# Kernel optimization log

Measured on AMD Instinct MI355X. Metric: run time of the kernel, lower is better.

Reference implementation:

```python
import jax, jax.numpy as jnp
import numpy as np

NS = [65536, 16384, 4096, 1024, 256, 64]          # nodes per level (64 = 8 graphs x 8 dense voxels)
ES = [1048576, 262144, 65536, 16384, 4096]        # edges per level (avg degree 16)
INS = [1, 15, 23, 31, 39]
OUTS = [12, 20, 28, 36, 44]
K = 5                                             # kernel_size


def setup_inputs():
    keys = iter(jax.random.split(jax.random.key(0), 64))
    d = {'x': jax.random.normal(next(keys), (NS[0], 1), jnp.float32),
         'pos': jax.random.uniform(next(keys), (NS[0], 3), jnp.float32)}
    for l in range(5):
        n, e, ci, co = NS[l], ES[l], INS[l], OUTS[l]
        d[f'src{l}'] = jax.random.randint(next(keys), (e,), 0, n)
        d[f'dst{l}'] = jax.random.randint(next(keys), (e,), 0, n)
        d[f'eattr{l}'] = jax.random.normal(next(keys), (e, 3), jnp.float32)
        d[f'cluster{l}'] = jax.random.randint(next(keys), (n,), 0, NS[l + 1])
        d[f'w1_{l}'] = jax.random.normal(next(keys), (3, K), jnp.float32) * 0.5
        d[f'b1_{l}'] = jnp.zeros((K,), jnp.float32)
        d[f'w2_{l}'] = jax.random.normal(next(keys), (K, ci * co), jnp.float32) / np.float32(np.sqrt(K * ci))
        d[f'b2_{l}'] = jnp.zeros((ci * co,), jnp.float32)
        d[f'root_{l}'] = jax.random.normal(next(keys), (ci, co), jnp.float32) / np.float32(np.sqrt(ci))
        d[f'bias_{l}'] = jnp.zeros((co,), jnp.float32)
    d['fc_w'] = jax.random.normal(next(keys), (8 * 47, 10), jnp.float32) / np.float32(np.sqrt(8 * 47))
    d['fc_b'] = jnp.zeros((10,), jnp.float32)
    return d


def _conv(x, src, dst, eattr, w1, b1, w2, b2, root, bias, n):
    # edge-conditioned kernel: MLP(edge_attr) -> [E, ci, co]
    h = jnp.tanh(eattr @ w1 + b1)                                  # [E, K]
    We = (h @ w2 + b2).reshape(eattr.shape[0], x.shape[1], -1)     # [E, ci, co]
    msg = jnp.einsum('ei,eio->eo', x[src], We)                     # gather + per-edge matvec
    s = jax.ops.segment_sum(msg, dst, num_segments=n)
    cnt = jax.ops.segment_sum(jnp.ones((dst.shape[0], 1), x.dtype), dst, num_segments=n)
    agg = s / jnp.maximum(cnt, 1.0)                                # mean aggregation
    return agg + x @ root + bias, jnp.mean(jnp.square(We))


def _pool(x, pos, cluster, n_next):
    # sparse voxel max pool on features, mean on positions; pos concatenated to features
    xm = jax.ops.segment_max(x, cluster, num_segments=n_next)
    xm = jnp.where(jnp.isfinite(xm), xm, 0.0)                      # empty voxels -> 0
    ps = jax.ops.segment_sum(pos, cluster, num_segments=n_next)
    cnt = jax.ops.segment_sum(jnp.ones((pos.shape[0], 1), pos.dtype), cluster, num_segments=n_next)
    pm = ps / jnp.maximum(cnt, 1.0)
    return jnp.concatenate([xm, pm], axis=1), pm


def reference(x, pos, src0, dst0, eattr0, cluster0, w1_0, b1_0, w2_0, b2_0, root_0, bias_0,
              src1, dst1, eattr1, cluster1, w1_1, b1_1, w2_1, b2_1, root_1, bias_1,
              src2, dst2, eattr2, cluster2, w1_2, b1_2, w2_2, b2_2, root_2, bias_2,
              src3, dst3, eattr3, cluster3, w1_3, b1_3, w2_3, b2_3, root_3, bias_3,
              src4, dst4, eattr4, cluster4, w1_4, b1_4, w2_4, b2_4, root_4, bias_4,
              fc_w, fc_b):
    lv = [(src0, dst0, eattr0, cluster0, w1_0, b1_0, w2_0, b2_0, root_0, bias_0),
          (src1, dst1, eattr1, cluster1, w1_1, b1_1, w2_1, b2_1, root_1, bias_1),
          (src2, dst2, eattr2, cluster2, w1_2, b1_2, w2_2, b2_2, root_2, bias_2),
          (src3, dst3, eattr3, cluster3, w1_3, b1_3, w2_3, b2_3, root_3, bias_3),
          (src4, dst4, eattr4, cluster4, w1_4, b1_4, w2_4, b2_4, root_4, bias_4)]
    closs = jnp.float32(0.0)
    for l, (src, dst, ea, cl, w1, b1, w2, b2, rt, bs) in enumerate(lv):
        x, c = _conv(x, src, dst, ea, w1, b1, w2, b2, rt, bs, NS[l])
        closs = closs + c
        x, pos = _pool(x, pos, cl, NS[l + 1])
    feat = x.reshape(-1, 8 * 47)                                   # [B, 8*47]
    logits = feat @ fc_w + fc_b
    return jax.nn.log_softmax(logits, axis=1), closs
```

## Files before the change

kernel.cpp:

```cpp
#include <hip/hip_runtime.h>
#include <hip/hip_fp16.h>
#include <math.h>


#define NBUCK 8
#define TILES0 256
#define NB0    512
#define IDXCAP 3072
#define TILES1 64
#define NB1    512

struct SegArgs {
    const int* idx[10];
    int*       cnt[10];
    int*       rp [10];
    int*       out[10];
    int        n  [10];
    int        nb [10];
    int        shift[10];
    int        tstart[11];
};

struct ScanAux {
    int* tilesum;
    int* tileoff;
    int  sstart[11];
    int  T;
};

struct HArgs {
    const float* eattr[5];
    const float* w1[5];
    const float* b1[5];
    float*       H;
    int          E[5];
    int          bstart[6];
};

struct WArgs {
    const float* w2[5];
    const float* b2[5];
    const float* H;
    float*       sq;
    int          cico[5];
    int          E[5];
};

__global__ __launch_bounds__(256) void countA_k(
    SegArgs a, HArgs ha, const int* __restrict__ dst0,
    const int* __restrict__ dst1, int* __restrict__ M, int* __restrict__ M1,
    int histBlocks)
{
    __shared__ int sh[NB0];
    int B = blockIdx.x;
    int t = threadIdx.x;

    if (B < TILES0) {
        for (int u = t; u < NB0; u += 256) sh[u] = 0;
        __syncthreads();
        int base = B * 4096 + t;
        #pragma unroll
        for (int it = 0; it < 16; it++)
            atomicAdd(&sh[dst0[base + it * 256] >> 7], 1);
        __syncthreads();
        for (int u = t; u < NB0; u += 256) M[(size_t)B * NB0 + u] = sh[u];
        return;
    }
    B -= TILES0;
    if (B < TILES1) {
        for (int u = t; u < NB1; u += 256) sh[u] = 0;
        __syncthreads();
        int base = B * 4096 + t;
        #pragma unroll
        for (int it = 0; it < 16; it++)
            atomicAdd(&sh[dst1[base + it * 256] >> 5], 1);
        __syncthreads();
        for (int u = t; u < NB1; u += 256) M1[(size_t)B * NB1 + u] = sh[u];
        return;
    }
    B -= TILES1;
    if (B < histBlocks) {
        int bucket = B % NBUCK;
        int T = B / NBUCK;
        int s = 0;
        while (s < 9 && T >= a.tstart[s + 1]) s++;
        int i = (T - a.tstart[s]) * 256 + t;
        if (i >= a.n[s]) return;
        int d = a.idx[s][i];
        if ((d >> a.shift[s]) != bucket) return;
        atomicAdd(&a.cnt[s][d], 1);
        return;
    }
    int b = B - histBlocks;
    const int K = 32;
    int l = 0;
    while (l < 4 && b >= ha.bstart[l + 1]) l++;
    int bloc = b - ha.bstart[l];
    const float* ea = ha.eattr[l];
    float w1r[15], b1r[5];
    #pragma unroll
    for (int i = 0; i < 15; i++) w1r[i] = ha.w1[l][i];
    #pragma unroll
    for (int i = 0; i < 5; i++)  b1r[i] = ha.b1[l][i];
    float acc[20];
    #pragma unroll
    for (int i = 0; i < 20; i++) acc[i] = 0.f;
    int base = bloc * 256 * K + t;
    for (int it = 0; it < K; it++) {
        int e = base + it * 256;
        if (e < ha.E[l]) {
            float e0 = ea[e * 3], e1 = ea[e * 3 + 1], e2 = ea[e * 3 + 2];
            float h[5];
            #pragma unroll
            for (int k = 0; k < 5; k++)
                h[k] = tanhf(e0 * w1r[k] + e1 * w1r[5 + k] + e2 * w1r[10 + k] + b1r[k]);
            int p = 5;
            #pragma unroll
            for (int k = 0; k < 5; k++) {
                acc[k] += h[k];
                #pragma unroll
                for (int k2 = k; k2 < 5; k2++) acc[p++] += h[k] * h[k2];
            }
        }
    }
    float* red = (float*)sh;
    int wid = t >> 6, lane = t & 63;
    #pragma unroll
    for (int v = 0; v < 20; v++) {
        float s = acc[v];
        #pragma unroll
        for (int o = 32; o; o >>= 1) s += __shfl_down(s, o);
        if (lane == 0) red[wid * 20 + v] = s;
    }
    __syncthreads();
    if (t < 20)
        atomicAdd(&ha.H[l * 20 + t],
                  red[t] + red[20 + t] + red[40 + t] + red[60 + t]);
}

__global__ __launch_bounds__(256) void scanP1_k(
    SegArgs a, ScanAux x, const int* __restrict__ M, int* __restrict__ M2,
    int* __restrict__ colTotal, const int* __restrict__ M1,
    int* __restrict__ M21, int* __restrict__ ct1)
{
    __shared__ int sc[256];
    int B = blockIdx.x;
    int t = threadIdx.x;

    if (B < NB0) {
        int v = M[(size_t)t * NB0 + B];
        sc[t] = v;
        __syncthreads();
        for (int d = 1; d < 256; d <<= 1) {
            int u = (t >= d) ? sc[t - d] : 0;
            __syncthreads();
            sc[t] += u;
            __syncthreads();
        }
        M2[(size_t)t * NB0 + B] = sc[t] - v;
        if (t == 255) colTotal[B] = sc[255];
        return;
    }
    B -= NB0;
    if (B < NB1) {
        if (t >= 64) return;
        int v = M1[(size_t)t * NB1 + B];
        int val = v;
        #pragma unroll
        for (int d = 1; d < 64; d <<= 1) {
            int u = __shfl_up(val, d);
            if (t >= d) val += u;
        }
        M21[(size_t)t * NB1 + B] = val - v;
        if (t == 63) ct1[B] = val;
        return;
    }
    int b = B - NB1;
    int s = 0;
    while (s < 9 && b >= x.sstart[s + 1]) s++;
    int tloc = b - x.sstart[s];
    int nb = a.nb[s];
    const int* cnt = a.cnt[s];
    int i0 = tloc * 4096 + t * 16;
    int sum = 0;
    #pragma unroll
    for (int k = 0; k < 16; k++) {
        int i = i0 + k;
        if (i < nb) sum += cnt[i];
    }
    #pragma unroll
    for (int o = 32; o; o >>= 1) sum += __shfl_down(sum, o);
    if ((t & 63) == 0) sc[t >> 6] = sum;
    __syncthreads();
    if (t == 0)
        x.tilesum[b] = sc[0] + sc[1] + sc[2] + sc[3];
}

__global__ __launch_bounds__(512) void scanP2_k(
    SegArgs a, ScanAux x, const int* __restrict__ colTotal,
    int* __restrict__ bucketStart, const int* __restrict__ ct1,
    int* __restrict__ bs1)
{
    __shared__ int sc[NB0];
    int t = threadIdx.x;
    if (blockIdx.x == 0) {
        int v = colTotal[t];
        sc[t] = v;
        __syncthreads();
        for (int d = 1; d < NB0; d <<= 1) {
            int u = (t >= d) ? sc[t - d] : 0;
            __syncthreads();
            sc[t] += u;
            __syncthreads();
        }
        bucketStart[t] = sc[t] - v;
        if (t == NB0 - 1) bucketStart[NB0] = sc[NB0 - 1];
        return;
    }
    if (blockIdx.x == 2) {
        int v = ct1[t];
        sc[t] = v;
        __syncthreads();
        for (int d = 1; d < NB1; d <<= 1) {
            int u = (t >= d) ? sc[t - d] : 0;
            __syncthreads();
            sc[t] += u;
            __syncthreads();
        }
        bs1[t] = sc[t] - v;
        if (t == NB1 - 1) bs1[NB1] = sc[NB1 - 1];
        return;
    }
    if (t >= 64) return;
    int lane = t;
    int orig = (lane < x.T) ? x.tilesum[lane] : 0;
    int val = orig;
    #pragma unroll
    for (int d = 1; d < 64; d <<= 1) {
        int v = __shfl_up(val, d);
        if (lane >= d) val += v;
    }
    int excl = val - orig;
    int s = 0;
    while (s < 9 && lane >= x.sstart[s + 1]) s++;
    int segExcl = __shfl(excl, x.sstart[s]);
    if (lane < x.T) {
        x.tileoff[lane] = excl - segExcl;
        if (lane == x.sstart[s + 1] - 1)
            a.rp[s][a.nb[s]] = val - segExcl;
    }
}

__global__ __launch_bounds__(256) void scanP3_k(
    SegArgs a, ScanAux x,
    const int* __restrict__ src, const int* __restrict__ dst,
    const float* __restrict__ ea, const float* __restrict__ x0,
    const int* __restrict__ M2, const int* __restrict__ bucketStart,
    float4* __restrict__ pay2,
    const float* __restrict__ w1, const float* __restrict__ b1,
    float* __restrict__ H0,
    const int* __restrict__ src1, const int* __restrict__ dst1,
    const float* __restrict__ ea1, const int* __restrict__ M21,
    const int* __restrict__ bs1, float4* __restrict__ pay1)
{
    __shared__ int   shi[NB0];
    __shared__ float shf[100];
    int B = blockIdx.x;
    int t = threadIdx.x;

    if (B < x.T) {
        int s = 0;
        while (s < 9 && B >= x.sstart[s + 1]) s++;
        int tloc = B - x.sstart[s];
        int nb = a.nb[s];
        const int* cnt = a.cnt[s];
        int* rp = a.rp[s];
        int i0 = tloc * 4096 + t * 16;
        int v[16];
        int sum = 0;
        #pragma unroll
        for (int k = 0; k < 16; k++) {
            int i = i0 + k;
            v[k] = (i < nb) ? cnt[i] : 0;
            sum += v[k];
        }
        int acc = sum;
        shi[t] = acc;
        __syncthreads();
        for (int d = 1; d < 256; d <<= 1) {
            int t2 = (t >= d) ? shi[t - d] : 0;
            __syncthreads();
            acc += t2;
            shi[t] = acc;
            __syncthreads();
        }
        int running = x.tileoff[B] + (acc - sum);
        #pragma unroll
        for (int k = 0; k < 16; k++) {
            int i = i0 + k;
            if (i < nb) rp[i] = running;
            running += v[k];
        }
        return;
    }
    B -= x.T;
    if (B < TILES0) {
        int tile = B;
        for (int u = t; u < NB0; u += 256)
            shi[u] = bucketStart[u] + M2[(size_t)tile * NB0 + u];
        if (t < 15) shf[t] = w1[t];
        if (t >= 32 && t < 37) shf[15 + t - 32] = b1[t - 32];
        __syncthreads();

        float acc[20];
        #pragma unroll
        for (int i = 0; i < 20; i++) acc[i] = 0.f;

        int base = tile * 4096 + t;
        #pragma unroll 4
        for (int it = 0; it < 16; it++) {
            int i = base + it * 256;
            int d = dst[i];
            float e0 = ea[i * 3], e1 = ea[i * 3 + 1], e2 = ea[i * 3 + 2];
            float h[5];
            #pragma unroll
            for (int k = 0; k < 5; k++)
                h[k] = tanhf(e0 * shf[k] + e1 * shf[5 + k] + e2 * shf[10 + k] + shf[15 + k]);
            int p = 5;
            #pragma unroll
            for (int k = 0; k < 5; k++) {
                acc[k] += h[k];
                #pragma unroll
                for (int k2 = k; k2 < 5; k2++) acc[p++] += h[k] * h[k2];
            }
            float xv = x0[src[i]];
            union HU { __half2 h2; float f; } p01, p23;
            p01.h2 = __floats2half2_rn(h[0], h[1]);
            p23.h2 = __floats2half2_rn(h[2], h[3]);
            unsigned wbits = ((unsigned)d << 16) |
                             (unsigned)__half_as_ushort(__float2half_rn(h[4]));
            int ps = atomicAdd(&shi[d >> 7], 1);
            pay2[ps] = make_float4(xv, p01.f, p23.f, __uint_as_float(wbits));
        }

        int wid = t >> 6, lane = t & 63;
        #pragma unroll
        for (int v = 0; v < 20; v++) {
            float s = acc[v];
            #pragma unroll
            for (int o = 32; o; o >>= 1) s += __shfl_down(s, o);
            if (lane == 0) shf[20 + wid * 20 + v] = s;
        }
        __syncthreads();
        if (t < 20)
            atomicAdd(&H0[t], shf[20 + t] + shf[40 + t] + shf[60 + t] + shf[80 + t]);
        return;
    }
    int tile = B - TILES0;
    for (int u = t; u < NB1; u += 256)
        shi[u] = bs1[u] + M21[(size_t)tile * NB1 + u];
    __syncthreads();
    int base = tile * 4096 + t;
    #pragma unroll 4
    for (int it = 0; it < 16; it++) {
        int i = base + it * 256;
        int d = dst1[i];
        int key = (d << 16) | src1[i];
        float e0 = ea1[i * 3], e1 = ea1[i * 3 + 1], e2 = ea1[i * 3 + 2];
        int ps = atomicAdd(&shi[d >> 5], 1);
        pay1[ps] = make_float4(__int_as_float(key), e0, e1, e2);
    }
}

__global__ __launch_bounds__(256) void scatC_k(
    SegArgs a, WArgs wa, int histBlocks,
    const float4* __restrict__ pay2, const int* __restrict__ bucketStart,
    const float* __restrict__ w2, const float* __restrict__ b2,
    const float* __restrict__ root, const float* __restrict__ bias,
    const float* __restrict__ x, float* __restrict__ y,
    const float4* __restrict__ pay1, const int* __restrict__ bs1,
    int* __restrict__ rp1, float4* __restrict__ rec1)
{
    __shared__ float wsm[96];
    __shared__ int hist[128], st[128], cur[128];
    __shared__ int idxL[IDXCAP];
    int B = blockIdx.x;
    int t = threadIdx.x;

    if (B < histBlocks) {
        int bucket = B % NBUCK;
        int T = B / NBUCK;
        int s = 0;
        while (s < 9 && T >= a.tstart[s + 1]) s++;
        int i = (T - a.tstart[s]) * 256 + t;
        if (i >= a.n[s]) return;
        int d = a.idx[s][i];
        if ((d >> a.shift[s]) != bucket) return;
        int p = atomicSub(&a.cnt[s][d], 1) - 1;
        a.out[s][a.rp[s][d] + p] = i;
        return;
    }
    B -= histBlocks;
    if (B < NB0) {
        if (t < 60) wsm[t] = w2[t];
        else if (t >= 64  && t < 76)  wsm[60 + t - 64]  = b2[t - 64];
        else if (t >= 128 && t < 140) wsm[72 + t - 128] = root[t - 128];
        else if (t >= 192 && t < 204) wsm[84 + t - 192] = bias[t - 192];
        if (t < 128) hist[t] = 0;
        __syncthreads();

        int lo = bucketStart[B], hi = bucketStart[B + 1];
        int bin0 = B << 7;
        const float* payw = (const float*)pay2;
        for (int j = lo + t; j < hi; j += 256) {
            int rel = (int)(__float_as_uint(payw[4 * j + 3]) >> 16) - bin0;
            atomicAdd(&hist[rel], 1);
        }
        __syncthreads();
        if (t < 128) st[t] = hist[t];
        __syncthreads();
        for (int d = 1; d < 128; d <<= 1) {
            int u = (t < 128 && t >= d) ? st[t - d] : 0;
            __syncthreads();
            if (t < 128) st[t] += u;
            __syncthreads();
        }
        if (t < 128) cur[t] = st[t] - hist[t];
        __syncthreads();
        for (int j = lo + t; j < hi; j += 256) {
            int rel = (int)(__float_as_uint(payw[4 * j + 3]) >> 16) - bin0;
            int p = atomicAdd(&cur[rel], 1);
            idxL[p] = j;
        }
        __syncthreads();

        if (t < 128) {
            int v = bin0 + t;
            int deg = hist[t];
            int s0 = st[t] - deg;
            float S0 = 0.f, S1 = 0.f, S2 = 0.f, S3 = 0.f, S4 = 0.f, S5 = 0.f;
            for (int jj = s0; jj < s0 + deg; jj++) {
                float4 R = pay2[idxL[jj]];
                union HU { float f; __half2 h2; } a01, a23;
                a01.f = R.y; a23.f = R.z;
                unsigned wbits = __float_as_uint(R.w);
                float xv = R.x;
                S0 += xv;
                S1 += __low2float(a01.h2)  * xv;
                S2 += __high2float(a01.h2) * xv;
                S3 += __low2float(a23.h2)  * xv;
                S4 += __high2float(a23.h2) * xv;
                S5 += __half2float(__ushort_as_half((unsigned short)(wbits & 0xffffu))) * xv;
            }
            float inv = 1.f / fmaxf((float)deg, 1.f);
            float xv = x[v];
            #pragma unroll
            for (int o = 0; o < 12; o++) {
                float msg = wsm[60 + o] * S0 + wsm[o] * S1 + wsm[12 + o] * S2 +
                            wsm[24 + o] * S3 + wsm[36 + o] * S4 + wsm[48 + o] * S5;
                y[v * 12 + o] = msg * inv + xv * wsm[72 + o] + wsm[84 + o];
            }
        }
        return;
    }
    B -= NB0;
    if (B < 5) {
        if (t >= 64) return;
        int l = B;
        const float* w2l = wa.w2[l];
        const float* b2l = wa.b2[l];
        int cico = wa.cico[l];
        float d[21];
        #pragma unroll
        for (int i = 0; i < 21; i++) d[i] = 0.f;
        for (int u = t; u < cico; u += 64) {
            float b = b2l[u];
            float w[5];
            #pragma unroll
            for (int k = 0; k < 5; k++) w[k] = w2l[k * cico + u];
            int p = 0;
            #pragma unroll
            for (int k = 0; k < 5; k++) {
                #pragma unroll
                for (int k2 = k; k2 < 5; k2++) d[p++] += w[k] * w[k2];
            }
            #pragma unroll
            for (int k = 0; k < 5; k++) d[15 + k] += b * w[k];
            d[20] += b * b;
        }
        #pragma unroll
        for (int i = 0; i < 21; i++) {
            #pragma unroll
            for (int off = 32; off; off >>= 1) d[i] += __shfl_down(d[i], off);
        }
        if (t == 0) {
            const float* H1 = wa.H + l * 20;
            const float* H2 = H1 + 5;
            float sq = (float)wa.E[l] * d[20];
            #pragma unroll
            for (int k = 0; k < 5; k++) sq += 2.f * d[15 + k] * H1[k];
            int p = 0;
            #pragma unroll
            for (int k = 0; k < 5; k++) {
                #pragma unroll
                for (int k2 = k; k2 < 5; k2++) {
                    sq += ((k == k2) ? 1.f : 2.f) * d[p] * H2[p];
                    p++;
                }
            }
            wa.sq[l] = sq;
        }
        return;
    }
    int b = B - 5;
    int lo = bs1[b], hi = bs1[b + 1];
    int bin0 = b << 5;
    if (t < 32) hist[t] = 0;
    __syncthreads();
    const float* payw = (const float*)pay1;
    for (int j = lo + t; j < hi; j += 256) {
        int rel = (int)(__float_as_uint(payw[4 * j]) >> 16) - bin0;
        atomicAdd(&hist[rel], 1);
    }
    __syncthreads();
    if (t < 32) {
        int v = hist[t];
        int val = v;
        #pragma unroll
        for (int d = 1; d < 32; d <<= 1) {
            int u = __shfl_up(val, d);
            if (t >= d) val += u;
        }
        st[t] = val - v;
        cur[t] = lo + val - v;
        rp1[bin0 + t] = lo + val - v;
        if (b == NB1 - 1 && t == 31) rp1[NB1 * 32] = hi;
    }
    __syncthreads();
    for (int j = lo + t; j < hi; j += 256) {
        float4 R = pay1[j];
        int rel = (int)(__float_as_uint(R.x) >> 16) - bin0;
        int p = atomicAdd(&cur[rel], 1);
        rec1[p] = R;
    }
}

__global__ __launch_bounds__(256) void conv1s_k(
    const int* __restrict__ rp, const float4* __restrict__ rec,
    const float* __restrict__ w1, const float* __restrict__ b1,
    const float* __restrict__ w2, const float* __restrict__ b2,
    const float* __restrict__ root, const float* __restrict__ bias,
    const float* __restrict__ x, float* __restrict__ y)
{
    constexpr int CI = 15, CO = 20, CH = 48, CICO = CI * CO;
    __shared__ float w1s[20];
    __shared__ float4 recb[CH];
    __shared__ int   svb[CH];
    __shared__ float hb[CH * 6];
    __shared__ float xs[CH * CI];
    __shared__ float S[6 * CI];

    int t = threadIdx.x;
    int v = blockIdx.x;
    if (t < 20) w1s[t] = (t < 15) ? w1[t] : b1[t - 15];
    int r0 = rp[v], r1 = rp[v + 1];
    int d  = r1 - r0;
    float acc = 0.f;

    for (int c0 = r0; c0 < r1; c0 += CH) {
        int cn = min(CH, r1 - c0);
        if (t < cn) {
            float4 R = rec[c0 + t];
            recb[t] = R;
            svb[t]  = (int)(__float_as_uint(R.x) & 0xffffu);
            hb[t * 6] = 1.f;
        }
        __syncthreads();
        if (t < cn * 5) {
            int j = t / 5, k = t % 5;
            float e0 = recb[j].y, e1 = recb[j].z, e2 = recb[j].w;
            hb[j * 6 + 1 + k] =
                tanhf(e0 * w1s[k] + e1 * w1s[5 + k] + e2 * w1s[10 + k] + w1s[15 + k]);
        }
        for (int u = t; u < cn * CI; u += 256)
            xs[u] = x[(size_t)svb[u / CI] * CI + (u % CI)];
        __syncthreads();
        if (t < 6 * CI) {
            int i = t / 6, k6 = t % 6;
            for (int j = 0; j < cn; j++)
                acc += hb[j * 6 + k6] * xs[j * CI + i];
        }
        __syncthreads();
    }

    if (t < 6 * CI) S[t] = acc;
    __syncthreads();

    if (t < CO) {
        float m = 0.f;
        for (int i = 0; i < CI; i++) {
            m += b2[i * CO + t] * S[i * 6];
            #pragma unroll
            for (int k = 0; k < 5; k++)
                m += w2[k * CICO + i * CO + t] * S[i * 6 + 1 + k];
        }
        m /= fmaxf((float)d, 1.f);
        for (int i = 0; i < CI; i++)
            m += x[(size_t)v * CI + i] * root[i * CO + t];
        y[(size_t)v * CO + t] = m + bias[t];
    }
}

template<int CI, int CO>
__global__ __launch_bounds__(256) void coop_conv_k(
    const int* __restrict__ rp, const int* __restrict__ eid,
    const int* __restrict__ src, const float* __restrict__ eattr,
    const float* __restrict__ w1, const float* __restrict__ b1,
    const float* __restrict__ w2, const float* __restrict__ b2,
    const float* __restrict__ root, const float* __restrict__ bias,
    const float* __restrict__ x, float* __restrict__ y)
{
    constexpr int CH   = 48;
    constexpr int CICO = CI * CO;
    __shared__ float w1s[20];
    __shared__ int   eb[CH], svb[CH];
    __shared__ float hb[CH * 6];
    __shared__ float xs[CH * CI];
    __shared__ float S[6 * CI];

    int t = threadIdx.x;
    int v = blockIdx.x;
    if (t < 20) w1s[t] = (t < 15) ? w1[t] : b1[t - 15];
    int r0 = rp[v], r1 = rp[v + 1];
    int d  = r1 - r0;
    float acc = 0.f;

    for (int c0 = r0; c0 < r1; c0 += CH) {
        int cn = min(CH, r1 - c0);
        if (t < cn) {
            int e = eid[c0 + t];
            eb[t]  = e;
            svb[t] = src[e];
            hb[t * 6] = 1.f;
        }
        __syncthreads();
        if (t < cn * 5) {
            int j = t / 5, k = t % 5;
            int e = eb[j];
            float e0 = eattr[e * 3], e1 = eattr[e * 3 + 1], e2 = eattr[e * 3 + 2];
            hb[j * 6 + 1 + k] =
                tanhf(e0 * w1s[k] + e1 * w1s[5 + k] + e2 * w1s[10 + k] + w1s[15 + k]);
        }
        for (int u = t; u < cn * CI; u += 256)
            xs[u] = x[(size_t)svb[u / CI] * CI + (u % CI)];
        __syncthreads();
        if (t < 6 * CI) {
            int i = t / 6, k6 = t % 6;
            for (int j = 0; j < cn; j++)
                acc += hb[j * 6 + k6] * xs[j * CI + i];
        }
        __syncthreads();
    }

    if (t < 6 * CI) S[t] = acc;
    __syncthreads();

    if (t < CO) {
        float m = 0.f;
        for (int i = 0; i < CI; i++) {
            m += b2[i * CO + t] * S[i * 6];
            #pragma unroll
            for (int k = 0; k < 5; k++)
                m += w2[k * CICO + i * CO + t] * S[i * 6 + 1 + k];
        }
        m /= fmaxf((float)d, 1.f);
        for (int i = 0; i < CI; i++)
            m += x[(size_t)v * CI + i] * root[i * CO + t];
        y[(size_t)v * CO + t] = m + bias[t];
    }
}

template<int CO>
__global__ __launch_bounds__(256) void pool_k(
    int NN,
    const int* __restrict__ crp, const int* __restrict__ cnid,
    const float* __restrict__ y, const float* __restrict__ pos,
    float* __restrict__ xn, float* __restrict__ pn)
{
    int t = blockIdx.x * 256 + threadIdx.x;
    if (t >= NN * (CO + 3)) return;
    int c = t / (CO + 3), o = t % (CO + 3);
    int r0 = crp[c], r1 = crp[c + 1];
    int d = r1 - r0;
    if (o < CO) {
        float m = -INFINITY;
        for (int j = r0; j < r1; j++)
            m = fmaxf(m, y[(size_t)cnid[j] * CO + o]);
        if (d == 0 || !isfinite(m)) m = 0.f;
        xn[c * (CO + 3) + o] = m;
    } else {
        int k = o - CO;
        float sum = 0.f;
        for (int j = r0; j < r1; j++)
            sum += pos[cnid[j] * 3 + k];
        float pm = sum / fmaxf((float)d, 1.f);
        xn[c * (CO + 3) + CO + k] = pm;
        pn[c * 3 + k] = pm;
    }
}

__global__ __launch_bounds__(128) void fc_k(
    const float* __restrict__ x5,
    const float* __restrict__ fc_w, const float* __restrict__ fc_b,
    const float* __restrict__ sq, float* __restrict__ out)
{
    __shared__ float feat[8 * 376];
    __shared__ float logit[80];
    __shared__ float roff[8];
    for (int t = threadIdx.x; t < 8 * 376; t += 128) feat[t] = x5[t];
    __syncthreads();
    int t = threadIdx.x;
    if (t < 80) {
        int b = t / 10, j = t % 10;
        float acc = fc_b[j];
        for (int k = 0; k < 376; k++) acc += feat[b * 376 + k] * fc_w[k * 10 + j];
        logit[t] = acc;
    }
    __syncthreads();
    if (t < 8) {
        float m = -1e30f;
        for (int j = 0; j < 10; j++) m = fmaxf(m, logit[t * 10 + j]);
        float ssum = 0.f;
        for (int j = 0; j < 10; j++) ssum += expf(logit[t * 10 + j] - m);
        roff[t] = m + logf(ssum);
    }
    __syncthreads();
    if (t < 80) out[t] = logit[t] - roff[t / 10];
    if (t == 0) {
        float closs = 0.f;
        closs += sq[0] * (1.0f / 12582912.0f);
        closs += sq[1] * (1.0f / 78643200.0f);
        closs += sq[2] * (1.0f / 42205184.0f);
        closs += sq[3] * (1.0f / 18284544.0f);
        closs += sq[4] * (1.0f / 7028736.0f);
        out[80] = closs;
    }
}


extern "C" void kernel_launch(void* const* d_in, const int* in_sizes, int n_in,
                              void* d_out, int out_size, void* d_ws, size_t ws_size,
                              hipStream_t stream)
{
    static const int NSa[6] = {65536, 16384, 4096, 1024, 256, 64};
    static const int ESa[5] = {1048576, 262144, 65536, 16384, 4096};
    static const int COa[5] = {12, 20, 28, 36, 44};
    static const int CIa[5] = {1, 15, 23, 31, 39};

    const float* x0   = (const float*)d_in[0];
    const float* pos0 = (const float*)d_in[1];

    int* wsw = (int*)d_ws;
    size_t off = 0;
    auto alw = [&](size_t n) -> size_t {
        size_t p = off; off += (n + 63) & ~(size_t)63; return p;
    };
    size_t degO[5], cdegO[5];
    for (int l = 2; l < 5; l++) degO[l]  = alw(NSa[l]);
    for (int l = 0; l < 5; l++) cdegO[l] = alw(NSa[l + 1]);
    size_t HO = alw(100);
    size_t zeroWords = off;
    size_t rpO[5], crpO[5], eidO[5], cnidO[5];
    rpO[1] = alw(NSa[1] + 1);
    for (int l = 2; l < 5; l++) rpO[l]  = alw(NSa[l] + 1);
    for (int l = 0; l < 5; l++) crpO[l] = alw(NSa[l + 1] + 1);
    for (int l = 2; l < 5; l++) eidO[l] = alw(ESa[l]);
    for (int l = 0; l < 5; l++) cnidO[l] = alw(NSa[l]);
    size_t tsO  = alw(64);
    size_t toO  = alw(64);
    size_t MO   = alw((size_t)TILES0 * NB0);
    size_t M2O  = alw((size_t)TILES0 * NB0);
    size_t ctO  = alw(NB0);
    size_t bsO  = alw(NB0 + 1);
    size_t payO = alw((size_t)ESa[0] * 4);
    size_t M1O  = alw((size_t)TILES1 * NB1);
    size_t M21O = alw((size_t)TILES1 * NB1);
    size_t ct1O = alw(NB1);
    size_t bs1O = alw(NB1 + 1);
    size_t pay1O = alw((size_t)ESa[1] * 4);
    size_t rec1O = alw((size_t)ESa[1] * 4);
    size_t yO   = alw((size_t)65536 * 12);
    size_t sqO  = alw(8);
    size_t xnO[5], pnO[5];
    for (int l = 0; l < 5; l++) xnO[l] = alw((size_t)NSa[l + 1] * (COa[l] + 3));
    for (int l = 0; l < 5; l++) pnO[l] = alw((size_t)NSa[l + 1] * 3);

    hipMemsetAsync(d_ws, 0, zeroWords * 4, stream);

    SegArgs sa{};
    int nseg = 0;
    for (int l = 2; l < 5; l++) {
        sa.idx[nseg] = (const int*)d_in[3 + 10 * l];
        sa.cnt[nseg] = wsw + degO[l];
        sa.rp [nseg] = wsw + rpO[l];
        sa.out[nseg] = wsw + eidO[l];
        sa.n  [nseg] = ESa[l];
        sa.nb [nseg] = NSa[l];
        nseg++;
    }
    for (int l = 0; l < 5; l++) {
        sa.idx[nseg] = (const int*)d_in[5 + 10 * l];
        sa.cnt[nseg] = wsw + cdegO[l];
        sa.rp [nseg] = wsw + crpO[l];
        sa.out[nseg] = wsw + cnidO[l];
        sa.n  [nseg] = NSa[l];
        sa.nb [nseg] = NSa[l + 1];
        nseg++;
    }
    ScanAux sx{};
    int tiles = 0, btiles = 0;
    for (int s = 0; s < nseg; s++) {
        int lg = 31 - __builtin_clz(sa.nb[s]);
        sa.shift[s] = lg - 3;
        sa.tstart[s] = tiles;
        tiles += (sa.n[s] + 255) / 256;
        sx.sstart[s] = btiles;
        btiles += (sa.nb[s] + 4095) / 4096;
    }
    for (int s = nseg; s <= 10; s++) {
        sa.tstart[s] = tiles;
        sx.sstart[s] = btiles;
        if (s < 10) {
            sa.idx[s] = sa.idx[nseg - 1]; sa.cnt[s] = sa.cnt[nseg - 1];
            sa.rp[s] = sa.rp[nseg - 1];   sa.out[s] = sa.out[nseg - 1];
            sa.n[s] = 0; sa.nb[s] = 8; sa.shift[s] = 0;
        }
    }
    sx.T = btiles;
    sx.tilesum = wsw + tsO;
    sx.tileoff = wsw + toO;
    int histBlocks = tiles * NBUCK;

    float4* pay2 = (float4*)(wsw + payO);
    float4* pay1 = (float4*)(wsw + pay1O);
    float4* rec1 = (float4*)(wsw + rec1O);
    float*  Hp   = (float*)(wsw + HO);

    HArgs ha{};
    int bs = 0;
    ha.bstart[0] = 0;
    ha.eattr[0] = (const float*)d_in[4];
    ha.w1[0] = (const float*)d_in[6];
    ha.b1[0] = (const float*)d_in[7];
    ha.E[0] = 0;
    for (int l = 1; l < 5; l++) {
        ha.eattr[l] = (const float*)d_in[4 + 10 * l];
        ha.w1[l]    = (const float*)d_in[6 + 10 * l];
        ha.b1[l]    = (const float*)d_in[7 + 10 * l];
        ha.E[l]     = ESa[l];
        ha.bstart[l] = bs;
        bs += (ESa[l] + 256 * 32 - 1) / (256 * 32);
    }
    ha.bstart[5] = bs;
    ha.H = Hp;

    WArgs wa{};
    for (int l = 0; l < 5; l++) {
        wa.w2[l]   = (const float*)d_in[8 + 10 * l];
        wa.b2[l]   = (const float*)d_in[9 + 10 * l];
        wa.cico[l] = CIa[l] * COa[l];
        wa.E[l]    = ESa[l];
    }
    wa.H  = Hp;
    wa.sq = (float*)(wsw + sqO);

    countA_k<<<TILES0 + TILES1 + histBlocks + bs, 256, 0, stream>>>(
        sa, ha, (const int*)d_in[3], (const int*)d_in[13],
        wsw + MO, wsw + M1O, histBlocks);
    scanP1_k<<<NB0 + NB1 + btiles, 256, 0, stream>>>(
        sa, sx, wsw + MO, wsw + M2O, wsw + ctO,
        wsw + M1O, wsw + M21O, wsw + ct1O);
    scanP2_k<<<3, 512, 0, stream>>>(sa, sx, wsw + ctO, wsw + bsO,
                                    wsw + ct1O, wsw + bs1O);
    scanP3_k<<<btiles + TILES0 + TILES1, 256, 0, stream>>>(
        sa, sx,
        (const int*)d_in[2], (const int*)d_in[3], (const float*)d_in[4],
        x0, wsw + M2O, wsw + bsO, pay2,
        (const float*)d_in[6], (const float*)d_in[7], Hp,
        (const int*)d_in[12], (const int*)d_in[13], (const float*)d_in[14],
        wsw + M21O, wsw + bs1O, pay1);

    float* yb = (float*)(wsw + yO);

    scatC_k<<<histBlocks + NB0 + 5 + NB1, 256, 0, stream>>>(
        sa, wa, histBlocks, pay2, wsw + bsO,
        (const float*)d_in[8], (const float*)d_in[9],
        (const float*)d_in[10], (const float*)d_in[11], x0, yb,
        pay1, wsw + bs1O, wsw + rpO[1], rec1);

    pool_k<12><<<(NSa[1] * 15 + 255) / 256, 256, 0, stream>>>(
        NSa[1], wsw + crpO[0], wsw + cnidO[0], yb, pos0,
        (float*)(wsw + xnO[0]), (float*)(wsw + pnO[0]));

    conv1s_k<<<NSa[1], 256, 0, stream>>>(
        wsw + rpO[1], rec1,
        (const float*)d_in[16], (const float*)d_in[17],
        (const float*)d_in[18], (const float*)d_in[19],
        (const float*)d_in[20], (const float*)d_in[21],
        (const float*)(wsw + xnO[0]), yb);
    pool_k<20><<<(NSa[2] * 23 + 255) / 256, 256, 0, stream>>>(
        NSa[2], wsw + crpO[1], wsw + cnidO[1], yb,
        (const float*)(wsw + pnO[0]),
        (float*)(wsw + xnO[1]), (float*)(wsw + pnO[1]));

#define LVLC(l, CI_, CO_) do {                                                 \
    const float* xin   = (const float*)(wsw + xnO[(l) - 1]);                   \
    const float* posin = (const float*)(wsw + pnO[(l) - 1]);                   \
    int N = NSa[(l)], NN = NSa[(l) + 1];                                       \
    coop_conv_k<CI_, CO_><<<N, 256, 0, stream>>>(                              \
        wsw + rpO[(l)], wsw + eidO[(l)],                                       \
        (const int*)d_in[2 + 10 * (l)], (const float*)d_in[4 + 10 * (l)],      \
        (const float*)d_in[6 + 10 * (l)], (const float*)d_in[7 + 10 * (l)],    \
        (const float*)d_in[8 + 10 * (l)], (const float*)d_in[9 + 10 * (l)],    \
        (const float*)d_in[10 + 10 * (l)], (const float*)d_in[11 + 10 * (l)],  \
        xin, yb);                                                              \
    pool_k<CO_><<<(NN * ((CO_) + 3) + 255) / 256, 256, 0, stream>>>(           \
        NN, wsw + crpO[(l)], wsw + cnidO[(l)], yb, posin,                      \
        (float*)(wsw + xnO[(l)]), (float*)(wsw + pnO[(l)]));                   \
} while (0)

    LVLC(2, 23, 28);
    LVLC(3, 31, 36);
    LVLC(4, 39, 44);
#undef LVLC

    fc_k<<<1, 128, 0, stream>>>((const float*)(wsw + xnO[4]),
                                (const float*)d_in[52], (const float*)d_in[53],
                                wa.sq, (float*)d_out);
}
```

Baseline: 416.5 us.

## Retile count/scatter phases, drop bucketed histograms, use LDS atomics for level-0 aggregation

Shrinks the per-block tiles in the level-0/1 bucket counting and payload scatter from 4096 to 1024 edges, giving more blocks, and makes the scan pass read four tile rows per thread. The 8-way bucket-filtered segment histogram and fill passes become a single pass with direct global atomics. Level-0 aggregation now accumulates straight into shared-memory float atomics instead of building a per-node local index list. tanhf is replaced by an exp-based fast tanh, and block orders inside the fused kernels are rearranged. These changes cut redundant reads and serial per-node loops, but they add atomic contention and make float summation order nondeterministic.

```diff
diff --git a/kernel.cpp b/kernel.cpp
--- a/kernel.cpp
+++ b/kernel.cpp
@@ -3,12 +3,17 @@
 #include <math.h>
 
 
-#define NBUCK 8
-#define TILES0 256
+#define TILES0 1024
+#define TSZ0   1024
 #define NB0    512
-#define IDXCAP 3072
-#define TILES1 64
+#define TILES1 256
+#define TSZ1   1024
 #define NB1    512
+
+__device__ __forceinline__ float ftanh(float x) {
+    float e = __expf(2.f * x);
+    return 1.f - 2.f / (e + 1.f);
+}
 
 struct SegArgs {
     const int* idx[10];
@@ -17,7 +22,6 @@
     int*       out[10];
     int        n  [10];
     int        nb [10];
-    int        shift[10];
     int        tstart[11];
 };
 
@@ -49,7 +53,7 @@
 __global__ __launch_bounds__(256) void countA_k(
     SegArgs a, HArgs ha, const int* __restrict__ dst0,
     const int* __restrict__ dst1, int* __restrict__ M, int* __restrict__ M1,
-    int histBlocks)
+    int hsBlocks)
 {
     __shared__ int sh[NB0];
     int B = blockIdx.x;
@@ -58,9 +62,9 @@
     if (B < TILES0) {
         for (int u = t; u < NB0; u += 256) sh[u] = 0;
         __syncthreads();
-        int base = B * 4096 + t;
-        #pragma unroll
-        for (int it = 0; it < 16; it++)
+        int base = B * TSZ0 + t;
+        #pragma unroll
+        for (int it = 0; it < 4; it++)
             atomicAdd(&sh[dst0[base + it * 256] >> 7], 1);
         __syncthreads();
         for (int u = t; u < NB0; u += 256) M[(size_t)B * NB0 + u] = sh[u];
@@ -70,72 +74,76 @@
     if (B < TILES1) {
         for (int u = t; u < NB1; u += 256) sh[u] = 0;
         __syncthreads();
-        int base = B * 4096 + t;
-        #pragma unroll
-        for (int it = 0; it < 16; it++)
+        int base = B * TSZ1 + t;
+        #pragma unroll
+        for (int it = 0; it < 4; it++)
             atomicAdd(&sh[dst1[base + it * 256] >> 5], 1);
         __syncthreads();
         for (int u = t; u < NB1; u += 256) M1[(size_t)B * NB1 + u] = sh[u];
         return;
     }
     B -= TILES1;
-    if (B < histBlocks) {
-        int bucket = B % NBUCK;
-        int T = B / NBUCK;
+    if (B < hsBlocks) {
+        const int K = 8;
+        int l = 0;
+        while (l < 4 && B >= ha.bstart[l + 1]) l++;
+        int bloc = B - ha.bstart[l];
+        const float* ea = ha.eattr[l];
+        float w1r[15], b1r[5];
+        #pragma unroll
+        for (int i = 0; i < 15; i++) w1r[i] = ha.w1[l][i];
+        #pragma unroll
+        for (int i = 0; i < 5; i++)  b1r[i] = ha.b1[l][i];
+        float acc[20];
+        #pragma unroll
+        for (int i = 0; i < 20; i++) acc[i] = 0.f;
+        int base = bloc * 256 * K + t;
+        for (int it = 0; it < K; it++) {
+            int e = base + it * 256;
+            if (e < ha.E[l]) {
+                float e0 = ea[e * 3], e1 = ea[e * 3 + 1], e2 = ea[e * 3 + 2];
+                float h[5];
+                #pragma unroll
+                for (int k = 0; k < 5; k++)
+                    h[k] = ftanh(e0 * w1r[k] + e1 * w1r[5 + k] + e2 * w1r[10 + k] + b1r[k]);
+                int p = 5;
+                #pragma unroll
+                for (int k = 0; k < 5; k++) {
+                    acc[k] += h[k];
+                    #pragma unroll
+                    for (int k2 = k; k2 < 5; k2++) acc[p++] += h[k] * h[k2];
+                }
+            }
+        }
+        float* red = (float*)sh;
+        int wid = t >> 6, lane = t & 63;
+        #pragma unroll
+        for (int v = 0; v < 20; v++) {
+            float s = acc[v];
+            #pragma unroll
+            for (int o = 32; o; o >>= 1) s += __shfl_down(s, o);
+            if (lane == 0) red[wid * 20 + v] = s;
+        }
+        __syncthreads();
+        if (t < 20)
+            atomicAdd(&ha.H[l * 20 + t],
+                      red[t] + red[20 + t] + red[40 + t] + red[60 + t]);
+        return;
+    }
+    B -= hsBlocks;
+    {
         int s = 0;
-        while (s < 9 && T >= a.tstart[s + 1]) s++;
-        int i = (T - a.tstart[s]) * 256 + t;
-        if (i >= a.n[s]) return;
-        int d = a.idx[s][i];
-        if ((d >> a.shift[s]) != bucket) return;
-        atomicAdd(&a.cnt[s][d], 1);
-        return;
-    }
-    int b = B - histBlocks;
-    const int K = 32;
-    int l = 0;
-    while (l < 4 && b >= ha.bstart[l + 1]) l++;
-    int bloc = b - ha.bstart[l];
-    const float* ea = ha.eattr[l];
-    float w1r[15], b1r[5];
-    #pragma unroll
-    for (int i = 0; i < 15; i++) w1r[i] = ha.w1[l][i];
-    #pragma unroll
-    for (int i = 0; i < 5; i++)  b1r[i] = ha.b1[l][i];
-    float acc[20];
-    #pragma unroll
-    for (int i = 0; i < 20; i++) acc[i] = 0.f;
-    int base = bloc * 256 * K + t;
-    for (int it = 0; it < K; it++) {
-        int e = base + it * 256;
-        if (e < ha.E[l]) {
-            float e0 = ea[e * 3], e1 = ea[e * 3 + 1], e2 = ea[e * 3 + 2];
-            float h[5];
-            #pragma unroll
-            for (int k = 0; k < 5; k++)
-                h[k] = tanhf(e0 * w1r[k] + e1 * w1r[5 + k] + e2 * w1r[10 + k] + b1r[k]);
-            int p = 5;
-            #pragma unroll
-            for (int k = 0; k < 5; k++) {
-                acc[k] += h[k];
-                #pragma unroll
-                for (int k2 = k; k2 < 5; k2++) acc[p++] += h[k] * h[k2];
-            }
-        }
-    }
-    float* red = (float*)sh;
-    int wid = t >> 6, lane = t & 63;
-    #pragma unroll
-    for (int v = 0; v < 20; v++) {
-        float s = acc[v];
-        #pragma unroll
-        for (int o = 32; o; o >>= 1) s += __shfl_down(s, o);
-        if (lane == 0) red[wid * 20 + v] = s;
-    }
-    __syncthreads();
-    if (t < 20)
-        atomicAdd(&ha.H[l * 20 + t],
-                  red[t] + red[20 + t] + red[40 + t] + red[60 + t]);
+        while (s < 9 && B >= a.tstart[s + 1]) s++;
+        int i0 = (B - a.tstart[s]) * 1024;
+        const int* idx = a.idx[s];
+        int* cnt = a.cnt[s];
+        int n = a.n[s];
+        #pragma unroll
+        for (int j = 0; j < 4; j++) {
+            int i = i0 + j * 256 + t;
+            if (i < n) atomicAdd(&cnt[idx[i]], 1);
+        }
+    }
 }
 
 __global__ __launch_bounds__(256) void scanP1_k(
@@ -148,8 +156,14 @@
     int t = threadIdx.x;
 
     if (B < NB0) {
-        int v = M[(size_t)t * NB0 + B];
-        sc[t] = v;
+        int v[4];
+        int s4 = 0;
+        #pragma unroll
+        for (int j = 0; j < 4; j++) {
+            v[j] = M[(size_t)(t * 4 + j) * NB0 + B];
+            s4 += v[j];
+        }
+        sc[t] = s4;
         __syncthreads();
         for (int d = 1; d < 256; d <<= 1) {
             int u = (t >= d) ? sc[t - d] : 0;
@@ -157,22 +171,28 @@
             sc[t] += u;
             __syncthreads();
         }
-        M2[(size_t)t * NB0 + B] = sc[t] - v;
+        int run = sc[t] - s4;
+        #pragma unroll
+        for (int j = 0; j < 4; j++) {
+            M2[(size_t)(t * 4 + j) * NB0 + B] = run;
+            run += v[j];
+        }
         if (t == 255) colTotal[B] = sc[255];
         return;
     }
     B -= NB0;
     if (B < NB1) {
-        if (t >= 64) return;
         int v = M1[(size_t)t * NB1 + B];
-        int val = v;
-        #pragma unroll
-        for (int d = 1; d < 64; d <<= 1) {
-            int u = __shfl_up(val, d);
-            if (t >= d) val += u;
-        }
-        M21[(size_t)t * NB1 + B] = val - v;
-        if (t == 63) ct1[B] = val;
+        sc[t] = v;
+        __syncthreads();
+        for (int d = 1; d < 256; d <<= 1) {
+            int u = (t >= d) ? sc[t - d] : 0;
+            __syncthreads();
+            sc[t] += u;
+            __syncthreads();
+        }
+        M21[(size_t)t * NB1 + B] = sc[t] - v;
+        if (t == 255) ct1[B] = sc[255];
         return;
     }
     int b = B - NB1;
@@ -268,42 +288,6 @@
     int B = blockIdx.x;
     int t = threadIdx.x;
 
-    if (B < x.T) {
-        int s = 0;
-        while (s < 9 && B >= x.sstart[s + 1]) s++;
-        int tloc = B - x.sstart[s];
-        int nb = a.nb[s];
-        const int* cnt = a.cnt[s];
-        int* rp = a.rp[s];
-        int i0 = tloc * 4096 + t * 16;
-        int v[16];
-        int sum = 0;
-        #pragma unroll
-        for (int k = 0; k < 16; k++) {
-            int i = i0 + k;
-            v[k] = (i < nb) ? cnt[i] : 0;
-            sum += v[k];
-        }
-        int acc = sum;
-        shi[t] = acc;
-        __syncthreads();
-        for (int d = 1; d < 256; d <<= 1) {
-            int t2 = (t >= d) ? shi[t - d] : 0;
-            __syncthreads();
-            acc += t2;
-            shi[t] = acc;
-            __syncthreads();
-        }
-        int running = x.tileoff[B] + (acc - sum);
-        #pragma unroll
-        for (int k = 0; k < 16; k++) {
-            int i = i0 + k;
-            if (i < nb) rp[i] = running;
-            running += v[k];
-        }
-        return;
-    }
-    B -= x.T;
     if (B < TILES0) {
         int tile = B;
         for (int u = t; u < NB0; u += 256)
@@ -316,16 +300,16 @@
         #pragma unroll
         for (int i = 0; i < 20; i++) acc[i] = 0.f;
 
-        int base = tile * 4096 + t;
-        #pragma unroll 4
-        for (int it = 0; it < 16; it++) {
+        int base = tile * TSZ0 + t;
+        #pragma unroll
+        for (int it = 0; it < 4; it++) {
             int i = base + it * 256;
             int d = dst[i];
             float e0 = ea[i * 3], e1 = ea[i * 3 + 1], e2 = ea[i * 3 + 2];
             float h[5];
             #pragma unroll
             for (int k = 0; k < 5; k++)
-                h[k] = tanhf(e0 * shf[k] + e1 * shf[5 + k] + e2 * shf[10 + k] + shf[15 + k]);
+                h[k] = ftanh(e0 * shf[k] + e1 * shf[5 + k] + e2 * shf[10 + k] + shf[15 + k]);
             int p = 5;
             #pragma unroll
             for (int k = 0; k < 5; k++) {
@@ -356,24 +340,61 @@
             atomicAdd(&H0[t], shf[20 + t] + shf[40 + t] + shf[60 + t] + shf[80 + t]);
         return;
     }
-    int tile = B - TILES0;
-    for (int u = t; u < NB1; u += 256)
-        shi[u] = bs1[u] + M21[(size_t)tile * NB1 + u];
+    B -= TILES0;
+    if (B < TILES1) {
+        int tile = B;
+        for (int u = t; u < NB1; u += 256)
+            shi[u] = bs1[u] + M21[(size_t)tile * NB1 + u];
+        __syncthreads();
+        int base = tile * TSZ1 + t;
+        #pragma unroll
+        for (int it = 0; it < 4; it++) {
+            int i = base + it * 256;
+            int d = dst1[i];
+            int key = (d << 16) | src1[i];
+            float e0 = ea1[i * 3], e1 = ea1[i * 3 + 1], e2 = ea1[i * 3 + 2];
+            int ps = atomicAdd(&shi[d >> 5], 1);
+            pay1[ps] = make_float4(__int_as_float(key), e0, e1, e2);
+        }
+        return;
+    }
+    B -= TILES1;
+    int s = 0;
+    while (s < 9 && B >= x.sstart[s + 1]) s++;
+    int tloc = B - x.sstart[s];
+    int nb = a.nb[s];
+    const int* cnt = a.cnt[s];
+    int* rp = a.rp[s];
+    int i0 = tloc * 4096 + t * 16;
+    int v[16];
+    int sum = 0;
+    #pragma unroll
+    for (int k = 0; k < 16; k++) {
+        int i = i0 + k;
+        v[k] = (i < nb) ? cnt[i] : 0;
+        sum += v[k];
+    }
+    int acc = sum;
+    shi[t] = acc;
     __syncthreads();
-    int base = tile * 4096 + t;
-    #pragma unroll 4
-    for (int it = 0; it < 16; it++) {
-        int i = base + it * 256;
-        int d = dst1[i];
-        int key = (d << 16) | src1[i];
-        float e0 = ea1[i * 3], e1 = ea1[i * 3 + 1], e2 = ea1[i * 3 + 2];
-        int ps = atomicAdd(&shi[d >> 5], 1);
-        pay1[ps] = make_float4(__int_as_float(key), e0, e1, e2);
+    for (int d = 1; d < 256; d <<= 1) {
+        int t2 = (t >= d) ? shi[t - d] : 0;
+        __syncthreads();
+        acc += t2;
+        shi[t] = acc;
+        __syncthreads();
+    }
+    int running = x.tileoff[B] + (acc - sum);
+    #pragma unroll
+    for (int k = 0; k < 16; k++) {
+        int i = i0 + k;
+        if (i < nb) rp[i] = running;
+        running += v[k];
     }
 }
 
 __global__ __launch_bounds__(256) void scatC_k(
-    SegArgs a, WArgs wa, int histBlocks,
+    SegArgs a, WArgs wa,
     const float4* __restrict__ pay2, const int* __restrict__ bucketStart,
     const float* __restrict__ w2, const float* __restrict__ b2,
     const float* __restrict__ root, const float* __restrict__ bias,
@@ -382,77 +403,45 @@
     int* __restrict__ rp1, float4* __restrict__ rec1)
 {
     __shared__ float wsm[96];
-    __shared__ int hist[128], st[128], cur[128];
-    __shared__ int idxL[IDXCAP];
+    __shared__ float nacc[7 * 128];
+    __shared__ int hist[32], st[32], cur[32];
     int B = blockIdx.x;
     int t = threadIdx.x;
 
-    if (B < histBlocks) {
-        int bucket = B % NBUCK;
-        int T = B / NBUCK;
-        int s = 0;
-        while (s < 9 && T >= a.tstart[s + 1]) s++;
-        int i = (T - a.tstart[s]) * 256 + t;
-        if (i >= a.n[s]) return;
-        int d = a.idx[s][i];
-        if ((d >> a.shift[s]) != bucket) return;
-        int p = atomicSub(&a.cnt[s][d], 1) - 1;
-        a.out[s][a.rp[s][d] + p] = i;
-        return;
-    }
-    B -= histBlocks;
     if (B < NB0) {
         if (t < 60) wsm[t] = w2[t];
         else if (t >= 64  && t < 76)  wsm[60 + t - 64]  = b2[t - 64];
         else if (t >= 128 && t < 140) wsm[72 + t - 128] = root[t - 128];
         else if (t >= 192 && t < 204) wsm[84 + t - 192] = bias[t - 192];
-        if (t < 128) hist[t] = 0;
+        for (int u = t; u < 7 * 128; u += 256) nacc[u] = 0.f;
         __syncthreads();
 
         int lo = bucketStart[B], hi = bucketStart[B + 1];
         int bin0 = B << 7;
-        const float* payw = (const float*)pay2;
         for (int j = lo + t; j < hi; j += 256) {
-            int rel = (int)(__float_as_uint(payw[4 * j + 3]) >> 16) - bin0;
-            atomicAdd(&hist[rel], 1);
-        }
-        __syncthreads();
-        if (t < 128) st[t] = hist[t];
-        __syncthreads();
-        for (int d = 1; d < 128; d <<= 1) {
-            int u = (t < 128 && t >= d) ? st[t - d] : 0;
-            __syncthreads();
-            if (t < 128) st[t] += u;
-            __syncthreads();
-        }
-        if (t < 128) cur[t] = st[t] - hist[t];
-        __syncthreads();
-        for (int j = lo + t; j < hi; j += 256) {
-            int rel = (int)(__float_as_uint(payw[4 * j + 3]) >> 16) - bin0;
-            int p = atomicAdd(&cur[rel], 1);
-            idxL[p] = j;
+            float4 R = pay2[j];
+            union HU { float f; __half2 h2; } a01, a23;
+            a01.f = R.y; a23.f = R.z;
+            unsigned wbits = __float_as_uint(R.w);
+            int node = (int)(wbits >> 16) - bin0;
+            float xv = R.x;
+            atomicAdd(&nacc[node], xv);
+            atomicAdd(&nacc[128 + node], __low2float(a01.h2)  * xv);
+            atomicAdd(&nacc[256 + node], __high2float(a01.h2) * xv);
+            atomicAdd(&nacc[384 + node], __low2float(a23.h2)  * xv);
+            atomicAdd(&nacc[512 + node], __high2float(a23.h2) * xv);
+            atomicAdd(&nacc[640 + node],
+                      __half2float(__ushort_as_half((unsigned short)(wbits & 0xffffu))) * xv);
+            atomicAdd(&nacc[768 + node], 1.f);
         }
         __syncthreads();
 
         if (t < 128) {
             int v = bin0 + t;
-            int deg = hist[t];
-            int s0 = st[t] - deg;
-            float S0 = 0.f, S1 = 0.f, S2 = 0.f, S3 = 0.f, S4 = 0.f, S5 = 0.f;
-            for (int jj = s0; jj < s0 + deg; jj++) {
-                float4 R = pay2[idxL[jj]];
-                union HU { float f; __half2 h2; } a01, a23;
-                a01.f = R.y; a23.f = R.z;
-                unsigned wbits = __float_as_uint(R.w);
-                float xv = R.x;
-                S0 += xv;
-                S1 += __low2float(a01.h2)  * xv;
-                S2 += __high2float(a01.h2) * xv;
-                S3 += __low2float(a23.h2)  * xv;
-                S4 += __high2float(a23.h2) * xv;
-                S5 += __half2float(__ushort_as_half((unsigned short)(wbits & 0xffffu))) * xv;
-            }
-            float inv = 1.f / fmaxf((float)deg, 1.f);
+            float deg = nacc[768 + t];
+            float S0 = nacc[t],       S1 = nacc[128 + t], S2 = nacc[256 + t];
+            float S3 = nacc[384 + t], S4 = nacc[512 + t], S5 = nacc[640 + t];
+            float inv = 1.f / fmaxf(deg, 1.f);
             float xv = x[v];
             #pragma unroll
             for (int o = 0; o < 12; o++) {
@@ -464,6 +453,41 @@
         return;
     }
     B -= NB0;
+    if (B < NB1) {
+        int b = B;
+        int lo = bs1[b], hi = bs1[b + 1];
+        int bin0 = b << 5;
+        if (t < 32) hist[t] = 0;
+        __syncthreads();
+        const float* payw = (const float*)pay1;
+        for (int j = lo + t; j < hi; j += 256) {
+            int rel = (int)(__float_as_uint(payw[4 * j]) >> 16) - bin0;
+            atomicAdd(&hist[rel], 1);
+        }
+        __syncthreads();
+        if (t < 32) {
+            int v = hist[t];
+            int val = v;
+            #pragma unroll
+            for (int d = 1; d < 32; d <<= 1) {
+                int u = __shfl_up(val, d);
+                if (t >= d) val += u;
+            }
+            st[t] = val - v;
+            cur[t] = lo + val - v;
+            rp1[bin0 + t] = lo + val - v;
+            if (b == NB1 - 1 && t == 31) rp1[NB1 * 32] = hi;
+        }
+        __syncthreads();
+        for (int j = lo + t; j < hi; j += 256) {
+            float4 R = pay1[j];
+            int rel = (int)(__float_as_uint(R.x) >> 16) - bin0;
+            int p = atomicAdd(&cur[rel], 1);
+            rec1[p] = R;
+        }
+        return;
+    }
+    B -= NB1;
     if (B < 5) {
         if (t >= 64) return;
         int l = B;
@@ -512,36 +536,25 @@
         }
         return;
     }
-    int b = B - 5;
-    int lo = bs1[b], hi = bs1[b + 1];
-    int bin0 = b << 5;
-    if (t < 32) hist[t] = 0;
-    __syncthreads();
-    const float* payw = (const float*)pay1;
-    for (int j = lo + t; j < hi; j += 256) {
-        int rel = (int)(__float_as_uint(payw[4 * j]) >> 16) - bin0;
-        atomicAdd(&hist[rel], 1);
-    }
-    __syncthreads();
-    if (t < 32) {
-        int v = hist[t];
-        int val = v;
-        #pragma unroll
-        for (int d = 1; d < 32; d <<= 1) {
-            int u = __shfl_up(val, d);
-            if (t >= d) val += u;
-        }
-        st[t] = val - v;
-        cur[t] = lo + val - v;
-        rp1[bin0 + t] = lo + val - v;
-        if (b == NB1 - 1 && t == 31) rp1[NB1 * 32] = hi;
-    }
-    __syncthreads();
-    for (int j = lo + t; j < hi; j += 256) {
-        float4 R = pay1[j];
-        int rel = (int)(__float_as_uint(R.x) >> 16) - bin0;
-        int p = atomicAdd(&cur[rel], 1);
-        rec1[p] = R;
+    B -= 5;
+    {
+        int s = 0;
+        while (s < 9 && B >= a.tstart[s + 1]) s++;
+        int i0 = (B - a.tstart[s]) * 1024;
+        const int* idx = a.idx[s];
+        int* cnt = a.cnt[s];
+        const int* rp = a.rp[s];
+        int* out = a.out[s];
+        int n = a.n[s];
+        #pragma unroll
+        for (int j = 0; j < 4; j++) {
+            int i = i0 + j * 256 + t;
+            if (i < n) {
+                int d = idx[i];
+                int p = atomicSub(&cnt[d], 1) - 1;
+                out[rp[d] + p] = i;
+            }
+        }
     }
 }
 
@@ -580,7 +593,7 @@
             int j = t / 5, k = t % 5;
             float e0 = recb[j].y, e1 = recb[j].z, e2 = recb[j].w;
             hb[j * 6 + 1 + k] =
-                tanhf(e0 * w1s[k] + e1 * w1s[5 + k] + e2 * w1s[10 + k] + w1s[15 + k]);
+                ftanh(e0 * w1s[k] + e1 * w1s[5 + k] + e2 * w1s[10 + k] + w1s[15 + k]);
         }
         for (int u = t; u < cn * CI; u += 256)
             xs[u] = x[(size_t)svb[u / CI] * CI + (u % CI)];
@@ -649,7 +662,7 @@
             int e = eb[j];
             float e0 = eattr[e * 3], e1 = eattr[e * 3 + 1], e2 = eattr[e * 3 + 2];
             hb[j * 6 + 1 + k] =
-                tanhf(e0 * w1s[k] + e1 * w1s[5 + k] + e2 * w1s[10 + k] + w1s[15 + k]);
+                ftanh(e0 * w1s[k] + e1 * w1s[5 + k] + e2 * w1s[10 + k] + w1s[15 + k]);
         }
         for (int u = t; u < cn * CI; u += 256)
             xs[u] = x[(size_t)svb[u / CI] * CI + (u % CI)];
@@ -793,6 +806,7 @@
     size_t sqO  = alw(8);
     size_t xnO[5], pnO[5];
     for (int l = 0; l < 5; l++) xnO[l] = alw((size_t)NSa[l + 1] * (COa[l] + 3));
+    for (int l = 0; l < 5; l++) pnO[l] = alw((size_t)NSa[l] * 3 / 4 + 64);
     for (int l = 0; l < 5; l++) pnO[l] = alw((size_t)NSa[l + 1] * 3);
 
     hipMemsetAsync(d_ws, 0, zeroWords * 4, stream);
@@ -820,10 +834,8 @@
     ScanAux sx{};
     int tiles = 0, btiles = 0;
     for (int s = 0; s < nseg; s++) {
-        int lg = 31 - __builtin_clz(sa.nb[s]);
-        sa.shift[s] = lg - 3;
         sa.tstart[s] = tiles;
-        tiles += (sa.n[s] + 255) / 256;
+        tiles += (sa.n[s] + 1023) / 1024;
         sx.sstart[s] = btiles;
         btiles += (sa.nb[s] + 4095) / 4096;
     }
@@ -833,13 +845,12 @@
         if (s < 10) {
             sa.idx[s] = sa.idx[nseg - 1]; sa.cnt[s] = sa.cnt[nseg - 1];
             sa.rp[s] = sa.rp[nseg - 1];   sa.out[s] = sa.out[nseg - 1];
-            sa.n[s] = 0; sa.nb[s] = 8; sa.shift[s] = 0;
+            sa.n[s] = 0; sa.nb[s] = 8;
         }
     }
     sx.T = btiles;
     sx.tilesum = wsw + tsO;
     sx.tileoff = wsw + toO;
-    int histBlocks = tiles * NBUCK;
 
     float4* pay2 = (float4*)(wsw + payO);
     float4* pay1 = (float4*)(wsw + pay1O);
@@ -859,7 +870,7 @@
         ha.b1[l]    = (const float*)d_in[7 + 10 * l];
         ha.E[l]     = ESa[l];
         ha.bstart[l] = bs;
-        bs += (ESa[l] + 256 * 32 - 1) / (256 * 32);
+        bs += (ESa[l] + 2047) / 2048;
     }
     ha.bstart[5] = bs;
     ha.H = Hp;
@@ -874,15 +885,15 @@
     wa.H  = Hp;
     wa.sq = (float*)(wsw + sqO);
 
-    countA_k<<<TILES0 + TILES1 + histBlocks + bs, 256, 0, stream>>>(
+    countA_k<<<TILES0 + TILES1 + bs + tiles, 256, 0, stream>>>(
         sa, ha, (const int*)d_in[3], (const int*)d_in[13],
-        wsw + MO, wsw + M1O, histBlocks);
+        wsw + MO, wsw + M1O, bs);
     scanP1_k<<<NB0 + NB1 + btiles, 256, 0, stream>>>(
         sa, sx, wsw + MO, wsw + M2O, wsw + ctO,
         wsw + M1O, wsw + M21O, wsw + ct1O);
     scanP2_k<<<3, 512, 0, stream>>>(sa, sx, wsw + ctO, wsw + bsO,
                                     wsw + ct1O, wsw + bs1O);
-    scanP3_k<<<btiles + TILES0 + TILES1, 256, 0, stream>>>(
+    scanP3_k<<<TILES0 + TILES1 + btiles, 256, 0, stream>>>(
         sa, sx,
         (const int*)d_in[2], (const int*)d_in[3], (const float*)d_in[4],
         x0, wsw + M2O, wsw + bsO, pay2,
@@ -892,8 +903,8 @@
 
     float* yb = (float*)(wsw + yO);
 
-    scatC_k<<<histBlocks + NB0 + 5 + NB1, 256, 0, stream>>>(
-        sa, wa, histBlocks, pay2, wsw + bsO,
+    scatC_k<<<NB0 + NB1 + 5 + tiles, 256, 0, stream>>>(
+        sa, wa, pay2, wsw + bsO,
         (const float*)d_in[8], (const float*)d_in[9],
         (const float*)d_in[10], (const float*)d_in[11], x0, yb,
         pay1, wsw + bs1O, wsw + rpO[1], rec1);
```

Measured after the change: 403.6 us. 3.1% less time.
